# Performance work log

Measured on AMD Instinct MI355X. Metric: run time of the kernel, lower is better.

Reference implementation:

```python
import jax, jax.numpy as jnp
import numpy as np

# ---- static synthetic forest: 64 complete binary trees, depth 9 (heap layout) ----
DEPTH = 9
N_TREES = 64
C = 8
M = 256
N_GEN = 8
NPT = 2 ** (DEPTH + 1) - 1          # 1023 nodes per tree
DIM = N_TREES * NPT                  # 65472 total nodes
_base = np.arange(N_TREES) * NPT

def _lvl_nodes(l):
    return (_base[:, None] + np.arange(2 ** l - 1, 2 ** (l + 1) - 1)[None, :]).reshape(-1)

LEVELS = []   # list of (parent_idx, child_idx) edge arrays, top level first
UPAR = []     # unique parents per level (== nodes of level l-1)
for _l in range(1, DEPTH + 1):
    _ch = np.arange(2 ** _l - 1, 2 ** (_l + 1) - 1)
    _pa = (_ch - 1) // 2
    LEVELS.append((jnp.asarray((_base[:, None] + _pa[None, :]).reshape(-1)),
                   jnp.asarray((_base[:, None] + _ch[None, :]).reshape(-1))))
    UPAR.append(jnp.asarray(_lvl_nodes(_l - 1)))
LEAVES = jnp.asarray(_lvl_nodes(DEPTH))
ROOTS = jnp.asarray(_base)
INTERNAL = jnp.asarray(np.concatenate([_lvl_nodes(l) for l in range(DEPTH)]))
TREES_IND = jnp.asarray(np.repeat(np.arange(N_TREES), NPT))
N_CH = 2.0  # every internal node has exactly 2 children -> segment mean = sum/2


def _forward(A, B, Pi, x):
    # softmax reparameterization (per generative head)
    sm_A = jax.nn.softmax(A, axis=0)          # (C,C,G), softmax over parent-state dim 0
    sm_B = jax.nn.softmax(B, axis=1)          # (C,M,G), softmax over symbols
    sm_Pi = jax.nn.softmax(Pi, axis=0)        # (C,G)

    # B[:, x] gathered per node, as (node, C, G)
    B_x = jnp.transpose(sm_B[:, x], (1, 0, 2))  # (DIM,C,G)

    # ---- reversed upward (leaves -> roots) ----
    beta = jnp.zeros((DIM, C, N_GEN), dtype=A.dtype)
    t_beta = jnp.zeros((DIM, C, N_GEN), dtype=A.dtype)
    b_leaf = sm_Pi[None, :, :] * B_x[LEAVES]                 # (L,C,G)
    beta = beta.at[LEAVES].set(b_leaf / b_leaf.sum(1, keepdims=True))
    for (pa, ch), upar in zip(reversed(LEVELS), reversed(UPAR)):
        beta_ch = beta[ch]                                   # (E,C,G)
        t_beta_ch = jnp.einsum('ijg,ejg->eig', sm_A, beta_ch)
        t_beta = t_beta + jax.ops.segment_sum(t_beta_ch, pa, num_segments=DIM) / N_CH
        beta_l = t_beta[upar] * B_x[upar]                    # (U,C,G)
        beta = beta.at[upar].set(beta_l / beta_l.sum(1, keepdims=True))

    # ---- reversed downward (roots -> leaves) ----
    eps = jnp.zeros((DIM, C, N_GEN), dtype=A.dtype)
    t_eps = jnp.zeros((DIM, C, C, N_GEN), dtype=A.dtype)
    eps = eps.at[ROOTS].set(beta[ROOTS])
    for pa, ch in LEVELS:
        # (E,Cpa,Cch,G)
        eps_joint = (eps[pa][:, :, None, :] * sm_A[None]
                     * beta[ch][:, None, :, :] / t_beta[pa][:, :, None, :])
        t_eps = t_eps + jax.ops.segment_sum(eps_joint, pa, num_segments=DIM) / N_CH
        eps = eps.at[ch].set(eps_joint.sum(1))

    # ---- log-likelihood ----
    lik = jnp.zeros((DIM, N_GEN), dtype=A.dtype)
    lik = lik.at[INTERNAL].add((t_eps[INTERNAL] * jnp.log(sm_A)[None]).sum((1, 2)))
    lik = lik + (eps * jnp.log(B_x)).sum(1)  # all_nodes == all nodes here
    lik = lik.at[LEAVES].add((eps[LEAVES] * jnp.log(sm_Pi)[None]).sum(1))
    ll = jax.ops.segment_sum(lik, TREES_IND, num_segments=N_TREES)  # (n_trees,G)
    return -ll


def setup_inputs() -> dict:
    key = jax.random.key(0)
    k1, k2, k3, k4 = jax.random.split(key, 4)
    A = jax.random.uniform(k1, (C, C, N_GEN), minval=-5.0, maxval=5.0)
    B = jax.random.uniform(k2, (C, M, N_GEN), minval=-5.0, maxval=5.0)
    Pi = jax.random.uniform(k3, (C, N_GEN), minval=-5.0, maxval=5.0)
    x = jax.random.randint(k4, (DIM,), 0, M)
    return {"A": A, "B": B, "Pi": Pi, "x": x}


def reference(A, B, Pi, x):
    return _forward(A, B, Pi, x)
```

## Files before the change

kernel.cpp:

```cpp
#include <hip/hip_runtime.h>

#define NT 256

namespace {
constexpr int C = 8, G = 8, M = 256, NPT = 1023;
constexpr int PD = 12;

__device__ __forceinline__ float rcpf(float x) { return __builtin_amdgcn_rcpf(x); }

__device__ __forceinline__ unsigned short f2b(float f) {
    union { float f; unsigned int u; } v; v.f = f;
    unsigned int r = v.u + 0x7FFFu + ((v.u >> 16) & 1u);
    return (unsigned short)(r >> 16);
}
__device__ __forceinline__ float2 up2(unsigned int p) {
    union { float f; unsigned int u; } a, b;
    a.u = (p & 0xFFFFu) << 16; b.u = p & 0xFFFF0000u;
    return make_float2(a.f, b.f);
}

#define LD8(dst, srcp) do {                                              \
    const float4 _a = *(const float4*)(srcp);                            \
    const float4 _b = *(const float4*)((srcp) + 4);                      \
    (dst)[0]=_a.x;(dst)[1]=_a.y;(dst)[2]=_a.z;(dst)[3]=_a.w;             \
    (dst)[4]=_b.x;(dst)[5]=_b.y;(dst)[6]=_b.z;(dst)[7]=_b.w; } while(0)

#define ST8(dstp, src) do {                                              \
    *(float4*)(dstp)       = make_float4((src)[0],(src)[1],(src)[2],(src)[3]); \
    *(float4*)((dstp) + 4) = make_float4((src)[4],(src)[5],(src)[6],(src)[7]); } while(0)

__global__ __launch_bounds__(NT, 2)
void htmm_fused(const float* __restrict__ Ag, const float* __restrict__ Bg,
                const float* __restrict__ Pig, const int* __restrict__ xg,
                float* __restrict__ out)
{
    __shared__ int xs[NPT + 1];
    __shared__ __align__(16) float smBt[M][PD];
    __shared__ __align__(16) float logBt[M][PD];
    __shared__ __align__(16) float bet[511][PD];
    __shared__ __align__(16) float tbe[255][PD];
    __shared__ __align__(16) float smA_s[C][C];
    __shared__ __align__(16) unsigned short alab[C][C];
    __shared__ float pi_s[2][C];
    __shared__ float red[4];

    const int tid  = threadIdx.x;
    const int wv   = tid >> 6, lane = tid & 63;
    const int tree = blockIdx.x >> 3, g = blockIdx.x & 7;

    for (int n = tid; n < NPT; n += NT) xs[n] = xg[tree * NPT + n];
    {
        const int i  = 2 * wv + (lane >> 5);
        const int c0 = lane & 31;
        float raw[8], ex[8], ssum = 0.f;
        #pragma unroll
        for (int t = 0; t < 8; ++t) {
            raw[t] = Bg[(i * M + c0 + 32 * t) * G + g];
            ex[t]  = __expf(raw[t]);
            ssum  += ex[t];
        }
        #pragma unroll
        for (int m = 1; m <= 16; m <<= 1) ssum += __shfl_xor(ssum, m);
        const float inv = rcpf(ssum), ls = __logf(ssum);
        #pragma unroll
        for (int t = 0; t < 8; ++t) {
            smBt [c0 + 32 * t][i] = ex[t] * inv;
            logBt[c0 + 32 * t][i] = raw[t] - ls;
        }
    }
    if (wv == 0) {
        const int si = lane >> 3, qj = lane & 7;
        const float raw = Ag[(si * C + qj) * G + g];
        float e = __expf(raw), S = e;
        #pragma unroll
        for (int m = 8; m <= 32; m <<= 1) S += __shfl_xor(S, m);
        const float v = e / S;
        smA_s[si][qj] = v;
        alab[si][qj]  = f2b(v * (raw - __logf(S)));
    } else if (wv == 1 && lane < C) {
        const float raw = Pig[lane * G + g];
        float e = __expf(raw), S = e;
        #pragma unroll
        for (int m = 1; m <= 4; m <<= 1) S += __shfl_xor(S, m);
        pi_s[0][lane] = e / S;
        pi_s[1][lane] = raw - __logf(S);
    }
    __syncthreads();

    unsigned int Apk[32];
    #pragma unroll
    for (int i = 0; i < 8; ++i) {
        float r[8]; LD8(r, &smA_s[i][0]);
        #pragma unroll
        for (int jj = 0; jj < 4; ++jj)
            Apk[i*4+jj] = (unsigned int)f2b(r[2*jj]) |
                          ((unsigned int)f2b(r[2*jj+1]) << 16);
    }

    auto trans_up = [&](const float* c8, float* tb) {
        #pragma unroll
        for (int i = 0; i < 8; ++i) {
            float t = 0.f;
            #pragma unroll
            for (int jj = 0; jj < 4; ++jj) {
                const float2 a = up2(Apk[i*4+jj]);
                t += a.x * c8[2*jj] + a.y * c8[2*jj+1];
            }
            tb[i] = 0.5f * t;
        }
    };
    auto wexp = [&](const float* w, float* es, float* ts) {
        #pragma unroll
        for (int j = 0; j < 8; ++j) { es[j] = 0.f; ts[j] = 0.f; }
        #pragma unroll
        for (int i = 0; i < 8; ++i) {
            #pragma unroll
            for (int jj = 0; jj < 4; ++jj) {
                const float2 a = up2(Apk[i*4+jj]);
                es[2*jj]   += w[i] * a.x;
                es[2*jj+1] += w[i] * a.y;
            }
            const uint4 lr = *(const uint4*)&alab[i][0];
            const float2 l0 = up2(lr.x), l1 = up2(lr.y), l2 = up2(lr.z), l3 = up2(lr.w);
            ts[0] += w[i]*l0.x; ts[1] += w[i]*l0.y;
            ts[2] += w[i]*l1.x; ts[3] += w[i]*l1.y;
            ts[4] += w[i]*l2.x; ts[5] += w[i]*l2.y;
            ts[6] += w[i]*l3.x; ts[7] += w[i]*l3.y;
        }
    };

    float acc = 0.f;

    const int nd8 = 255 + tid;
    const int xv8 = xs[nd8], xvL = xs[2*nd8 + 1], xvR = xs[2*nd8 + 2];
    float bl0[8], bl1[8], tb8[8], b8[8];
    {
        float piR[8]; LD8(piR, &pi_s[0][0]);
        float sm[8], u[8], S, inv;
        LD8(sm, &smBt[xvL][0]);
        S = 0.f;
        #pragma unroll
        for (int i = 0; i < 8; ++i) { u[i] = piR[i] * sm[i]; S += u[i]; }
        inv = rcpf(S);
        #pragma unroll
        for (int i = 0; i < 8; ++i) bl0[i] = u[i] * inv;

        LD8(sm, &smBt[xvR][0]);
        S = 0.f;
        #pragma unroll
        for (int i = 0; i < 8; ++i) { u[i] = piR[i] * sm[i]; S += u[i]; }
        inv = rcpf(S);
        #pragma unroll
        for (int i = 0; i < 8; ++i) bl1[i] = u[i] * inv;

        float c[8];
        #pragma unroll
        for (int j = 0; j < 8; ++j) c[j] = bl0[j] + bl1[j];
        trans_up(c, tb8);
        LD8(sm, &smBt[xv8][0]);
        S = 0.f;
        #pragma unroll
        for (int i = 0; i < 8; ++i) { u[i] = tb8[i] * sm[i]; S += u[i]; }
        inv = rcpf(S);
        #pragma unroll
        for (int i = 0; i < 8; ++i) b8[i] = u[i] * inv;
        ST8(&bet[nd8][0], b8);
    }
    __syncthreads();

    for (int lvl = 7; lvl >= 0; --lvl) {
        const int cnt = 1 << lvl, base = cnt - 1;
        if (tid < cnt) {
            const int p = base + tid, cl = 2*p + 1;
            float lb_[8], rb_[8], cb[8], tb[8];
            LD8(lb_, &bet[cl][0]);
            LD8(rb_, &bet[cl + 1][0]);
            #pragma unroll
            for (int j = 0; j < 8; ++j) cb[j] = lb_[j] + rb_[j];
            trans_up(cb, tb);
            ST8(&tbe[p][0], tb);
            float sm[8], u[8], S = 0.f;
            LD8(sm, &smBt[xs[p]][0]);
            #pragma unroll
            for (int i = 0; i < 8; ++i) { u[i] = tb[i] * sm[i]; S += u[i]; }
            const float inv = rcpf(S);
            float b[8];
            #pragma unroll
            for (int i = 0; i < 8; ++i) b[i] = u[i] * inv;
            ST8(&bet[p][0], b);
        }
        __syncthreads();
    }

    if (tid == 0) {
        float b0[8], lb[8];
        LD8(b0, &bet[0][0]);
        LD8(lb, &logBt[xs[0]][0]);
        #pragma unroll
        for (int j = 0; j < 8; ++j) acc += b0[j] * lb[j];
    }

    for (int dc = 1; dc <= 7; ++dc) {
        const int cntp = 1 << (dc - 1), basep = cntp - 1;
        if (tid < cntp) {
            const int p = basep + tid;
            float ep[8], tp[8], w[8], es[8], ts[8];
            LD8(ep, &bet[p][0]);
            LD8(tp, &tbe[p][0]);
            #pragma unroll
            for (int i = 0; i < 8; ++i) w[i] = ep[i] * rcpf(tp[i]);
            wexp(w, es, ts);
            #pragma unroll
            for (int cc = 0; cc < 2; ++cc) {
                const int ch = 2*p + 1 + cc;
                float bc[8], lb[8], ev[8];
                LD8(bc, &bet[ch][0]);
                LD8(lb, &logBt[xs[ch]][0]);
                float a1 = 0.f, a2 = 0.f;
                #pragma unroll
                for (int j = 0; j < 8; ++j) {
                    ev[j] = bc[j] * es[j];
                    a1 += bc[j] * ts[j];
                    a2 += ev[j] * lb[j];
                }
                acc += 0.5f * a1 + a2;
                ST8(&bet[ch][0], ev);
            }
        }
        __syncthreads();
    }

    {
        const int p7 = (nd8 - 1) >> 1;
        float ep[8], tp[8], w[8], es[8], ts[8];
        LD8(ep, &bet[p7][0]);
        LD8(tp, &tbe[p7][0]);
        #pragma unroll
        for (int i = 0; i < 8; ++i) w[i] = ep[i] * rcpf(tp[i]);
        wexp(w, es, ts);

        float lb[8], ev8[8], w8[8];
        LD8(lb, &logBt[xv8][0]);
        float a1 = 0.f, a2 = 0.f;
        #pragma unroll
        for (int j = 0; j < 8; ++j) {
            ev8[j] = b8[j] * es[j];
            a1 += b8[j] * ts[j];
            a2 += ev8[j] * lb[j];
        }
        acc += 0.5f * a1 + a2;
        #pragma unroll
        for (int i = 0; i < 8; ++i) w8[i] = ev8[i] * rcpf(tb8[i]);

        wexp(w8, es, ts);
        float lPi[8]; LD8(lPi, &pi_s[1][0]);
        LD8(lb, &logBt[xvL][0]);
        a1 = 0.f; a2 = 0.f;
        #pragma unroll
        for (int j = 0; j < 8; ++j) {
            const float ev = bl0[j] * es[j];
            a1 += bl0[j] * ts[j];
            a2 += ev * (lb[j] + lPi[j]);
        }
        acc += 0.5f * a1 + a2;
        LD8(lb, &logBt[xvR][0]);
        a1 = 0.f; a2 = 0.f;
        #pragma unroll
        for (int j = 0; j < 8; ++j) {
            const float ev = bl1[j] * es[j];
            a1 += bl1[j] * ts[j];
            a2 += ev * (lb[j] + lPi[j]);
        }
        acc += 0.5f * a1 + a2;
    }

    #pragma unroll
    for (int m = 1; m <= 32; m <<= 1) acc += __shfl_xor(acc, m);
    if (lane == 0) red[wv] = acc;
    __syncthreads();
    if (tid == 0) out[blockIdx.x] = -(red[0] + red[1] + red[2] + red[3]);
}
}

extern "C" void kernel_launch(void* const* d_in, const int* in_sizes, int n_in,
                              void* d_out, int out_size, void* d_ws, size_t ws_size,
                              hipStream_t stream) {
    const float* A  = (const float*)d_in[0];
    const float* Bm = (const float*)d_in[1];
    const float* Pi = (const float*)d_in[2];
    const int*   x  = (const int*)d_in[3];
    float* o = (float*)d_out;
    hipLaunchKernelGGL(htmm_fused, dim3(64 * 8), dim3(NT), 0, stream,
                       A, Bm, Pi, x, o);
}
```

Before: 76.83 us.

## Double block size to one thread per leaf with shuffle-based sibling exchange

Raises the block to 512 threads so each thread owns one leaf instead of a pair. Sibling sums and level-8 downward weights are exchanged with lane shuffles, and only even lanes handle level-8 nodes. The B softmax setup is remapped to one wave per state. This adds parallelism to the leaf-heavy phases, at the cost of more threads idling in the upper tree levels and more barrier cost per block.

```diff
diff --git a/kernel.cpp b/kernel.cpp
--- a/kernel.cpp
+++ b/kernel.cpp
@@ -1,6 +1,6 @@
 #include <hip/hip_runtime.h>
 
-#define NT 256
+#define NT 512
 
 namespace {
 constexpr int C = 8, G = 8, M = 256, NPT = 1023;
@@ -29,7 +29,7 @@
     *(float4*)(dstp)       = make_float4((src)[0],(src)[1],(src)[2],(src)[3]); \
     *(float4*)((dstp) + 4) = make_float4((src)[4],(src)[5],(src)[6],(src)[7]); } while(0)
 
-__global__ __launch_bounds__(NT, 2)
+__global__ __launch_bounds__(NT, 4)
 void htmm_fused(const float* __restrict__ Ag, const float* __restrict__ Bg,
                 const float* __restrict__ Pig, const int* __restrict__ xg,
                 float* __restrict__ out)
@@ -42,7 +42,7 @@
     __shared__ __align__(16) float smA_s[C][C];
     __shared__ __align__(16) unsigned short alab[C][C];
     __shared__ float pi_s[2][C];
-    __shared__ float red[4];
+    __shared__ float red[8];
 
     const int tid  = threadIdx.x;
     const int wv   = tid >> 6, lane = tid & 63;
@@ -50,22 +50,23 @@
 
     for (int n = tid; n < NPT; n += NT) xs[n] = xg[tree * NPT + n];
     {
-        const int i  = 2 * wv + (lane >> 5);
-        const int c0 = lane & 31;
-        float raw[8], ex[8], ssum = 0.f;
-        #pragma unroll
-        for (int t = 0; t < 8; ++t) {
-            raw[t] = Bg[(i * M + c0 + 32 * t) * G + g];
+        const int i = wv;
+        float raw[4], ex[4], ssum = 0.f;
+        #pragma unroll
+        for (int t = 0; t < 4; ++t) {
+            const int c = lane + 64 * t;
+            raw[t] = Bg[(i * M + c) * G + g];
             ex[t]  = __expf(raw[t]);
             ssum  += ex[t];
         }
         #pragma unroll
-        for (int m = 1; m <= 16; m <<= 1) ssum += __shfl_xor(ssum, m);
+        for (int m = 1; m <= 32; m <<= 1) ssum += __shfl_xor(ssum, m);
         const float inv = rcpf(ssum), ls = __logf(ssum);
         #pragma unroll
-        for (int t = 0; t < 8; ++t) {
-            smBt [c0 + 32 * t][i] = ex[t] * inv;
-            logBt[c0 + 32 * t][i] = raw[t] - ls;
+        for (int t = 0; t < 4; ++t) {
+            const int c = lane + 64 * t;
+            smBt [c][i] = ex[t] * inv;
+            logBt[c][i] = raw[t] - ls;
         }
     }
     if (wv == 0) {
@@ -131,40 +132,34 @@
 
     float acc = 0.f;
 
-    const int nd8 = 255 + tid;
-    const int xv8 = xs[nd8], xvL = xs[2*nd8 + 1], xvR = xs[2*nd8 + 2];
-    float bl0[8], bl1[8], tb8[8], b8[8];
+    const int nl  = 511 + tid;
+    const int xvL = xs[nl];
+    const int n8  = 255 + (tid >> 1);
+    float bl[8], b8[8], tb8[8];
     {
         float piR[8]; LD8(piR, &pi_s[0][0]);
-        float sm[8], u[8], S, inv;
+        float sm[8], u[8], S = 0.f;
         LD8(sm, &smBt[xvL][0]);
-        S = 0.f;
         #pragma unroll
         for (int i = 0; i < 8; ++i) { u[i] = piR[i] * sm[i]; S += u[i]; }
-        inv = rcpf(S);
-        #pragma unroll
-        for (int i = 0; i < 8; ++i) bl0[i] = u[i] * inv;
-
-        LD8(sm, &smBt[xvR][0]);
-        S = 0.f;
-        #pragma unroll
-        for (int i = 0; i < 8; ++i) { u[i] = piR[i] * sm[i]; S += u[i]; }
-        inv = rcpf(S);
-        #pragma unroll
-        for (int i = 0; i < 8; ++i) bl1[i] = u[i] * inv;
-
-        float c[8];
-        #pragma unroll
-        for (int j = 0; j < 8; ++j) c[j] = bl0[j] + bl1[j];
-        trans_up(c, tb8);
-        LD8(sm, &smBt[xv8][0]);
-        S = 0.f;
-        #pragma unroll
-        for (int i = 0; i < 8; ++i) { u[i] = tb8[i] * sm[i]; S += u[i]; }
-        inv = rcpf(S);
-        #pragma unroll
-        for (int i = 0; i < 8; ++i) b8[i] = u[i] * inv;
-        ST8(&bet[nd8][0], b8);
+        const float inv = rcpf(S);
+        #pragma unroll
+        for (int i = 0; i < 8; ++i) bl[i] = u[i] * inv;
+
+        float c8[8];
+        #pragma unroll
+        for (int j = 0; j < 8; ++j) c8[j] = bl[j] + __shfl_xor(bl[j], 1);
+        if ((tid & 1) == 0) {
+            trans_up(c8, tb8);
+            float sm2[8], u2[8], S2 = 0.f;
+            LD8(sm2, &smBt[xs[n8]][0]);
+            #pragma unroll
+            for (int i = 0; i < 8; ++i) { u2[i] = tb8[i] * sm2[i]; S2 += u2[i]; }
+            const float inv2 = rcpf(S2);
+            #pragma unroll
+            for (int i = 0; i < 8; ++i) b8[i] = u2[i] * inv2;
+            ST8(&bet[n8][0], b8);
+        }
     }
     __syncthreads();
 
@@ -231,44 +226,41 @@
     }
 
     {
-        const int p7 = (nd8 - 1) >> 1;
-        float ep[8], tp[8], w[8], es[8], ts[8];
-        LD8(ep, &bet[p7][0]);
-        LD8(tp, &tbe[p7][0]);
-        #pragma unroll
-        for (int i = 0; i < 8; ++i) w[i] = ep[i] * rcpf(tp[i]);
-        wexp(w, es, ts);
-
-        float lb[8], ev8[8], w8[8];
-        LD8(lb, &logBt[xv8][0]);
+        float w8[8];
+        if ((tid & 1) == 0) {
+            const int p7 = (n8 - 1) >> 1;
+            float ep[8], tp[8], w[8], es[8], ts[8];
+            LD8(ep, &bet[p7][0]);
+            LD8(tp, &tbe[p7][0]);
+            #pragma unroll
+            for (int i = 0; i < 8; ++i) w[i] = ep[i] * rcpf(tp[i]);
+            wexp(w, es, ts);
+            float lb[8], ev8[8];
+            LD8(lb, &logBt[xs[n8]][0]);
+            float a1 = 0.f, a2 = 0.f;
+            #pragma unroll
+            for (int j = 0; j < 8; ++j) {
+                ev8[j] = b8[j] * es[j];
+                a1 += b8[j] * ts[j];
+                a2 += ev8[j] * lb[j];
+            }
+            acc += 0.5f * a1 + a2;
+            #pragma unroll
+            for (int i = 0; i < 8; ++i) w8[i] = ev8[i] * rcpf(tb8[i]);
+        }
+        #pragma unroll
+        for (int i = 0; i < 8; ++i) w8[i] = __shfl(w8[i], lane & 62);
+
+        float es2[8], ts2[8];
+        wexp(w8, es2, ts2);
+        float lPi[8]; LD8(lPi, &pi_s[1][0]);
+        float lb[8];
+        LD8(lb, &logBt[xvL][0]);
         float a1 = 0.f, a2 = 0.f;
         #pragma unroll
         for (int j = 0; j < 8; ++j) {
-            ev8[j] = b8[j] * es[j];
-            a1 += b8[j] * ts[j];
-            a2 += ev8[j] * lb[j];
-        }
-        acc += 0.5f * a1 + a2;
-        #pragma unroll
-        for (int i = 0; i < 8; ++i) w8[i] = ev8[i] * rcpf(tb8[i]);
-
-        wexp(w8, es, ts);
-        float lPi[8]; LD8(lPi, &pi_s[1][0]);
-        LD8(lb, &logBt[xvL][0]);
-        a1 = 0.f; a2 = 0.f;
-        #pragma unroll
-        for (int j = 0; j < 8; ++j) {
-            const float ev = bl0[j] * es[j];
-            a1 += bl0[j] * ts[j];
-            a2 += ev * (lb[j] + lPi[j]);
-        }
-        acc += 0.5f * a1 + a2;
-        LD8(lb, &logBt[xvR][0]);
-        a1 = 0.f; a2 = 0.f;
-        #pragma unroll
-        for (int j = 0; j < 8; ++j) {
-            const float ev = bl1[j] * es[j];
-            a1 += bl1[j] * ts[j];
+            const float ev = bl[j] * es2[j];
+            a1 += bl[j] * ts2[j];
             a2 += ev * (lb[j] + lPi[j]);
         }
         acc += 0.5f * a1 + a2;
@@ -278,7 +270,12 @@
     for (int m = 1; m <= 32; m <<= 1) acc += __shfl_xor(acc, m);
     if (lane == 0) red[wv] = acc;
     __syncthreads();
-    if (tid == 0) out[blockIdx.x] = -(red[0] + red[1] + red[2] + red[3]);
+    if (tid == 0) {
+        float s = 0.f;
+        #pragma unroll
+        for (int i = 0; i < 8; ++i) s += red[i];
+        out[blockIdx.x] = -s;
+    }
 }
 }
 
```

Result: slower. 100.1 us (+30.2%).
